# Kernel tuning notes

Hardware: AMD Instinct MI355X
Metric: run time of the kernel (lower is better)

The kernel has to match this reference:

```python
import jax, jax.numpy as jnp
import numpy as np

B, S, H = 4, 2048, 1024
NH, HD = 16, 64
WIN = 64  # window_size = min(64, seq_len)
SCALE = float(np.sqrt(HD))


def setup_inputs() -> dict:
    key = jax.random.key(0)
    ks = jax.random.split(key, 10)
    w = lambda k, shp: (jax.random.normal(k, shp, jnp.float32) * 0.02)
    return {
        "x": jax.random.normal(ks[0], (B, S, H), jnp.float32),
        "attention_mask": jnp.ones((B, S), jnp.int32),
        "Wq": w(ks[1], (H, NH * HD)), "bq": jnp.zeros((NH * HD,), jnp.float32),
        "Wk": w(ks[2], (H, NH * HD)), "bk": jnp.zeros((NH * HD,), jnp.float32),
        "Wv": w(ks[3], (H, NH * HD)), "bv": jnp.zeros((NH * HD,), jnp.float32),
        "Wo": w(ks[4], (NH * HD, H)), "bo": jnp.zeros((H,), jnp.float32),
    }


def reference(x, attention_mask, Wq, bq, Wk, bk, Wv, bv, Wo, bo):
    # projections -> [B, NH, S, HD]
    def split_heads(t):
        return t.reshape(B, S, NH, HD).transpose(0, 2, 1, 3)
    q = split_heads(x @ Wq + bq)
    k = split_heads(x @ Wk + bk)
    v = split_heads(x @ Wv + bv)

    scores = jnp.einsum("bhqd,bhkd->bhqk", q, k) / SCALE  # [B,NH,S,S]

    # local banded mask: |i - j| <= window_size // 2
    idx = jnp.arange(S)
    local = jnp.abs(idx[None, :] - idx[:, None]) <= (WIN // 2)  # [S,S]
    scores = jnp.where(local[None, None, :, :], scores, -jnp.inf)

    # padding mask: [B,1,1,S]
    scores = jnp.where(attention_mask[:, None, None, :] == 0, -jnp.inf, scores)

    probs = jax.nn.softmax(scores, axis=-1)
    probs = jnp.nan_to_num(probs)  # rows that are fully masked -> 0

    out = jnp.einsum("bhqk,bhkd->bhqd", probs, v)
    out = out.transpose(0, 2, 1, 3).reshape(B, S, NH * HD)
    return out @ Wo + bo
```

## Files before the change

kernel.cpp:

```cpp
#include <hip/hip_runtime.h>
#include <stdint.h>

typedef unsigned short u16;
typedef __attribute__((ext_vector_type(8))) short short8;
typedef __attribute__((ext_vector_type(4))) float f32x4;

#define S_LEN 2048
#define HID   1024
#define QKV_LD 3072
#define M_ROWS 8192

__device__ __forceinline__ u16 f2bf(float f) {
  unsigned u = __float_as_uint(f);
  unsigned r = (u + 0x7fffu + ((u >> 16) & 1u)) >> 16;
  return (u16)r;
}

__device__ __forceinline__ void gload16(const u16* g, u16* l) {
  __builtin_amdgcn_global_load_lds(
      (const __attribute__((address_space(1))) unsigned int*)(g),
      (__attribute__((address_space(3))) unsigned int*)(l),
      16, 0, 0);
}

__global__ __launch_bounds__(256) void cvt_f32_to_bf16(
    const float* __restrict__ in, u16* __restrict__ out, int n) {
  int i = (blockIdx.x * 256 + threadIdx.x) * 8;
  if (i + 8 > n) return;
  float4 a = *(const float4*)(in + i);
  float4 b = *(const float4*)(in + i + 4);
  u16 t[8];
  t[0] = f2bf(a.x); t[1] = f2bf(a.y); t[2] = f2bf(a.z); t[3] = f2bf(a.w);
  t[4] = f2bf(b.x); t[5] = f2bf(b.y); t[6] = f2bf(b.z); t[7] = f2bf(b.w);
  *(short8*)(out + i) = *(short8*)t;
}

__global__ __launch_bounds__(256) void transpose_to_bf16(
    const float* __restrict__ in, u16* __restrict__ out, int K, int N) {
  __shared__ float tile[32][33];
  int tx = threadIdx.x & 31, ty = threadIdx.x >> 5;
  int n0 = blockIdx.x * 32, k0 = blockIdx.y * 32;
#pragma unroll
  for (int i = 0; i < 32; i += 8)
    tile[ty + i][tx] = in[(size_t)(k0 + ty + i) * N + n0 + tx];
  __syncthreads();
#pragma unroll
  for (int i = 0; i < 32; i += 8)
    out[(size_t)(n0 + ty + i) * K + k0 + tx] = f2bf(tile[tx][ty + i]);
}

__global__ __launch_bounds__(256) void pack_bias(
    const float* __restrict__ bq, const float* __restrict__ bk,
    const float* __restrict__ bv, float* __restrict__ out) {
  int i = blockIdx.x * 256 + threadIdx.x;
  if (i >= 3072) return;
  out[i] = (i < 1024) ? bq[i] : (i < 2048) ? bk[i - 1024] : bv[i - 2048];
}

template<int OUT_BF16>
__global__ __launch_bounds__(256, 2) void gemm_bt(
    const u16* __restrict__ A, const u16* __restrict__ Bt,
    const float* __restrict__ bias, void* __restrict__ Cout,
    int M, int N, int K) {
  __shared__ __align__(16) u16 Al[128 * 64];
  __shared__ __align__(16) u16 Bl[128 * 64];
  const int tid = threadIdx.x;
  const int wave = tid >> 6, lane = tid & 63;
  const int nbn = N >> 7;
  int wg = blockIdx.x;
  const int cpx = (int)gridDim.x >> 3;
  wg = (wg & 7) * cpx + (wg >> 3);
  const int bm = wg / nbn, bn = wg % nbn;

  const int wm = wave >> 1, wn = wave & 1;
  const int lrow = lane >> 3;
  const int lslot = lane & 7;
  const int gslot = lslot ^ lrow;
  const int qlane = lane & 15, kgrp = lane >> 4;

  size_t a_off[4], b_off[4];
  u16 *al_base[4], *bl_base[4];
#pragma unroll
  for (int t = 0; t < 4; ++t) {
    int rr = (wave * 4 + t) * 8 + lrow;
    a_off[t] = (size_t)(bm * 128 + rr) * K + gslot * 8;
    b_off[t] = (size_t)(bn * 128 + rr) * K + gslot * 8;
    al_base[t] = Al + (wave * 4 + t) * 512;
    bl_base[t] = Bl + (wave * 4 + t) * 512;
  }

  f32x4 acc[4][4] = {};
  for (int kt = 0; kt < K; kt += 64) {
#pragma unroll
    for (int t = 0; t < 4; ++t) {
      gload16(A + a_off[t] + kt, al_base[t]);
      gload16(Bt + b_off[t] + kt, bl_base[t]);
    }
    __syncthreads();
#pragma unroll
    for (int kk = 0; kk < 2; ++kk) {
      short8 af[4], bf[4];
#pragma unroll
      for (int mf = 0; mf < 4; ++mf) {
        int row = wm * 64 + mf * 16 + qlane;
        int s = (kk * 4 + kgrp) ^ (row & 7);
        af[mf] = *(const short8*)&Al[row * 64 + s * 8];
      }
#pragma unroll
      for (int nf = 0; nf < 4; ++nf) {
        int row = wn * 64 + nf * 16 + qlane;
        int s = (kk * 4 + kgrp) ^ (row & 7);
        bf[nf] = *(const short8*)&Bl[row * 64 + s * 8];
      }
#pragma unroll
      for (int mf = 0; mf < 4; ++mf)
#pragma unroll
        for (int nf = 0; nf < 4; ++nf)
          acc[mf][nf] = __builtin_amdgcn_mfma_f32_16x16x32_bf16(
              af[mf], bf[nf], acc[mf][nf], 0, 0, 0);
    }
    __syncthreads();
  }

#pragma unroll
  for (int nf = 0; nf < 4; ++nf) {
    int col = bn * 128 + wn * 64 + nf * 16 + qlane;
    float bv = bias[col];
#pragma unroll
    for (int mf = 0; mf < 4; ++mf) {
      int row0 = bm * 128 + wm * 64 + mf * 16 + kgrp * 4;
#pragma unroll
      for (int r = 0; r < 4; ++r) {
        float v = acc[mf][nf][r] + bv;
        if (OUT_BF16)
          ((u16*)Cout)[(size_t)(row0 + r) * N + col] = f2bf(v);
        else
          ((float*)Cout)[(size_t)(row0 + r) * N + col] = v;
      }
    }
  }
}

__global__ __launch_bounds__(256, 2) void attn_local(
    const u16* __restrict__ qkv, const int* __restrict__ amask,
    u16* __restrict__ aout) {
  __shared__ __align__(16) u16 Kl[192][72];
  __shared__ __align__(16) u16 Vt[64][200];
  __shared__ __align__(16) u16 Pl[4][32][104];

  const int tid = threadIdx.x, wave = tid >> 6, lane = tid & 63;
  const int qlane = lane & 15, kgrp = lane >> 4;
  const int bz = blockIdx.x;
  const int qt = bz & 15, h = (bz >> 4) & 15, b = bz >> 8;
  const int qs0 = qt * 128;
  const int jt = qs0 - 32;
  const size_t rbase = (size_t)b * S_LEN;

  {
    const int r0 = tid >> 3, c0 = (tid & 7) * 8;
#pragma unroll
    for (int p = 0; p < 6; ++p) {
      int row = p * 32 + r0;
      int j = jt + row;
      u16 kv[8], vv[8];
      if (j >= 0 && j < S_LEN) {
        const u16* kp = qkv + (rbase + j) * QKV_LD + HID + h * 64 + c0;
        *(short8*)kv = *(const short8*)kp;
        *(short8*)vv = *(const short8*)(kp + HID);
      } else {
#pragma unroll
        for (int q = 0; q < 8; ++q) { kv[q] = 0; vv[q] = 0; }
      }
      *(short8*)&Kl[row][c0] = *(short8*)kv;
#pragma unroll
      for (int q = 0; q < 8; ++q) Vt[c0 + q][row] = vv[q];
    }
  }

  short8 qf[2][2];
#pragma unroll
  for (int mf = 0; mf < 2; ++mf)
#pragma unroll
    for (int kk = 0; kk < 2; ++kk)
      qf[mf][kk] = *(const short8*)(qkv +
          (rbase + qs0 + wave * 32 + mf * 16 + qlane) * QKV_LD +
          h * 64 + kk * 32 + kgrp * 8);

  __syncthreads();

  f32x4 sc[2][6] = {};
#pragma unroll
  for (int kk = 0; kk < 2; ++kk) {
    short8 kf[6];
#pragma unroll
    for (int nf = 0; nf < 6; ++nf)
      kf[nf] = *(const short8*)&Kl[wave * 32 + nf * 16 + qlane][kk * 32 + kgrp * 8];
#pragma unroll
    for (int mf = 0; mf < 2; ++mf)
#pragma unroll
      for (int nf = 0; nf < 6; ++nf)
        sc[mf][nf] = __builtin_amdgcn_mfma_f32_16x16x32_bf16(
            qf[mf][kk], kf[nf], sc[mf][nf], 0, 0, 0);
  }

  int jcol[6], mv[6];
#pragma unroll
  for (int nf = 0; nf < 6; ++nf) {
    int j = jt + wave * 32 + nf * 16 + qlane;
    jcol[nf] = j;
    mv[nf] = (j >= 0 && j < S_LEN) ? amask[rbase + j] : 0;
  }

  float inv[2][4];
#pragma unroll
  for (int mf = 0; mf < 2; ++mf) {
    const int irow0 = qs0 + wave * 32 + mf * 16 + kgrp * 4;
    float mx[4] = {-1e30f, -1e30f, -1e30f, -1e30f};
#pragma unroll
    for (int r = 0; r < 4; ++r) {
      int i = irow0 + r;
#pragma unroll
      for (int nf = 0; nf < 6; ++nf) {
        int d = i - jcol[nf];
        if (mv[nf] && d >= -32 && d <= 32) mx[r] = fmaxf(mx[r], sc[mf][nf][r]);
      }
    }
#pragma unroll
    for (int m = 1; m < 16; m <<= 1)
#pragma unroll
      for (int r = 0; r < 4; ++r)
        mx[r] = fmaxf(mx[r], __shfl_xor(mx[r], m));
    float sm[4] = {0.f, 0.f, 0.f, 0.f};
#pragma unroll
    for (int r = 0; r < 4; ++r) {
      int i = irow0 + r;
#pragma unroll
      for (int nf = 0; nf < 6; ++nf) {
        int d = i - jcol[nf];
        bool val = mv[nf] && d >= -32 && d <= 32;
        float p = val ? __expf((sc[mf][nf][r] - mx[r]) * 0.125f) : 0.f;
        sc[mf][nf][r] = p;
        sm[r] += p;
      }
    }
#pragma unroll
    for (int m = 1; m < 16; m <<= 1)
#pragma unroll
      for (int r = 0; r < 4; ++r)
        sm[r] += __shfl_xor(sm[r], m);
#pragma unroll
    for (int r = 0; r < 4; ++r)
      inv[mf][r] = sm[r] > 0.f ? 1.f / sm[r] : 0.f;
#pragma unroll
    for (int nf = 0; nf < 6; ++nf)
#pragma unroll
      for (int r = 0; r < 4; ++r)
        Pl[wave][mf * 16 + kgrp * 4 + r][nf * 16 + qlane] = f2bf(sc[mf][nf][r]);
  }
  __syncthreads();

  f32x4 oc[2][4] = {};
#pragma unroll
  for (int ks = 0; ks < 3; ++ks) {
    short8 pa[2], vb[4];
#pragma unroll
    for (int mf = 0; mf < 2; ++mf)
      pa[mf] = *(const short8*)&Pl[wave][mf * 16 + qlane][ks * 32 + kgrp * 8];
#pragma unroll
    for (int nf = 0; nf < 4; ++nf)
      vb[nf] = *(const short8*)&Vt[nf * 16 + qlane][wave * 32 + ks * 32 + kgrp * 8];
#pragma unroll
    for (int mf = 0; mf < 2; ++mf)
#pragma unroll
      for (int nf = 0; nf < 4; ++nf)
        oc[mf][nf] = __builtin_amdgcn_mfma_f32_16x16x32_bf16(
            pa[mf], vb[nf], oc[mf][nf], 0, 0, 0);
  }

#pragma unroll
  for (int mf = 0; mf < 2; ++mf)
#pragma unroll
    for (int nf = 0; nf < 4; ++nf)
#pragma unroll
      for (int r = 0; r < 4; ++r) {
        size_t row = rbase + qs0 + wave * 32 + mf * 16 + kgrp * 4 + r;
        aout[row * HID + h * 64 + nf * 16 + qlane] =
            f2bf(oc[mf][nf][r] * inv[mf][r]);
      }
}

extern "C" void kernel_launch(void* const* d_in, const int* in_sizes, int n_in,
                              void* d_out, int out_size, void* d_ws, size_t ws_size,
                              hipStream_t stream) {
  const float* x  = (const float*)d_in[0];
  const int* amask = (const int*)d_in[1];
  const float* Wq = (const float*)d_in[2];
  const float* bq = (const float*)d_in[3];
  const float* Wk = (const float*)d_in[4];
  const float* bk = (const float*)d_in[5];
  const float* Wv = (const float*)d_in[6];
  const float* bv = (const float*)d_in[7];
  const float* Wo = (const float*)d_in[8];
  const float* bo = (const float*)d_in[9];
  float* out = (float*)d_out;

  char* w = (char*)d_ws;
  u16* xb    = (u16*)w;   w += (size_t)M_ROWS * HID * 2;
  u16* wqkvt = (u16*)w;   w += (size_t)3072 * 1024 * 2;
  u16* wot   = (u16*)w;   w += (size_t)1024 * 1024 * 2;
  float* bqkv = (float*)w; w += 3072 * 4 + 256;
  u16* qkv   = (u16*)w;   w += (size_t)M_ROWS * 3072 * 2;
  u16* aout  = (u16*)w;   w += (size_t)M_ROWS * HID * 2;

  cvt_f32_to_bf16<<<4096, 256, 0, stream>>>(x, xb, M_ROWS * HID);
  dim3 tg(32, 32);
  transpose_to_bf16<<<tg, 256, 0, stream>>>(Wq, wqkvt,                1024, 1024);
  transpose_to_bf16<<<tg, 256, 0, stream>>>(Wk, wqkvt + 1024 * 1024,  1024, 1024);
  transpose_to_bf16<<<tg, 256, 0, stream>>>(Wv, wqkvt + 2048 * 1024,  1024, 1024);
  transpose_to_bf16<<<tg, 256, 0, stream>>>(Wo, wot,                  1024, 1024);
  pack_bias<<<12, 256, 0, stream>>>(bq, bk, bv, bqkv);

  gemm_bt<1><<<64 * 24, 256, 0, stream>>>(xb, wqkvt, bqkv, qkv, M_ROWS, 3072, 1024);
  attn_local<<<1024, 256, 0, stream>>>(qkv, amask, aout);
  gemm_bt<0><<<64 * 8, 256, 0, stream>>>(aout, wot, bo, out, M_ROWS, 1024, 1024);
}
```

Measured before the change: 131.7 us.

## Add specialised 256x384-tile QKV GEMM and merge preprocessing kernel launches

Replaces the generic QKV projection GEMM with a dedicated kernel that uses 512 threads, a 256x384 output tile, and a triple-buffered LDS pipeline with swizzled addressing and MFMA priority hints. This raises data reuse per block and overlaps global loads with compute. It also merges the four weight transposes into one 3D-grid launch and folds bias packing into the conversion kernel, cutting launch overhead. The 256-block grid fills the GPU in a single wave, which may leave compute units idle, and a large register footprint risks spills.

```diff
diff --git a/kernel.cpp b/kernel.cpp
--- a/kernel.cpp
+++ b/kernel.cpp
@@ -23,10 +23,22 @@
       16, 0, 0);
 }
 
-__global__ __launch_bounds__(256) void cvt_f32_to_bf16(
-    const float* __restrict__ in, u16* __restrict__ out, int n) {
+__device__ __forceinline__ void wgbar() {
+  asm volatile("" ::: "memory");
+  __builtin_amdgcn_s_barrier();
+  asm volatile("" ::: "memory");
+}
+
+__global__ __launch_bounds__(256) void cvt_bias(
+    const float* __restrict__ in, u16* __restrict__ out, int n,
+    const float* __restrict__ bq, const float* __restrict__ bk,
+    const float* __restrict__ bv, float* __restrict__ bqkv) {
+  if (blockIdx.x == (unsigned)(n / (256 * 8))) {
+    for (int i = threadIdx.x; i < 3072; i += 256)
+      bqkv[i] = (i < 1024) ? bq[i] : (i < 2048) ? bk[i - 1024] : bv[i - 2048];
+    return;
+  }
   int i = (blockIdx.x * 256 + threadIdx.x) * 8;
-  if (i + 8 > n) return;
   float4 a = *(const float4*)(in + i);
   float4 b = *(const float4*)(in + i + 4);
   u16 t[8];
@@ -35,26 +47,126 @@
   *(short8*)(out + i) = *(short8*)t;
 }
 
-__global__ __launch_bounds__(256) void transpose_to_bf16(
-    const float* __restrict__ in, u16* __restrict__ out, int K, int N) {
+__global__ __launch_bounds__(256) void pack_weights(
+    const float* __restrict__ Wq, const float* __restrict__ Wk,
+    const float* __restrict__ Wv, const float* __restrict__ Wo,
+    u16* __restrict__ wqkvt, u16* __restrict__ wot) {
   __shared__ float tile[32][33];
+  const int z = blockIdx.z;
+  const float* in = (z == 0) ? Wq : (z == 1) ? Wk : (z == 2) ? Wv : Wo;
+  u16* out = (z < 3) ? (wqkvt + (size_t)z * 1024 * 1024) : wot;
   int tx = threadIdx.x & 31, ty = threadIdx.x >> 5;
   int n0 = blockIdx.x * 32, k0 = blockIdx.y * 32;
 #pragma unroll
   for (int i = 0; i < 32; i += 8)
-    tile[ty + i][tx] = in[(size_t)(k0 + ty + i) * N + n0 + tx];
+    tile[ty + i][tx] = in[(size_t)(k0 + ty + i) * 1024 + n0 + tx];
   __syncthreads();
 #pragma unroll
   for (int i = 0; i < 32; i += 8)
-    out[(size_t)(n0 + ty + i) * K + k0 + tx] = f2bf(tile[tx][ty + i]);
-}
-
-__global__ __launch_bounds__(256) void pack_bias(
-    const float* __restrict__ bq, const float* __restrict__ bk,
-    const float* __restrict__ bv, float* __restrict__ out) {
-  int i = blockIdx.x * 256 + threadIdx.x;
-  if (i >= 3072) return;
-  out[i] = (i < 1024) ? bq[i] : (i < 2048) ? bk[i - 1024] : bv[i - 2048];
+    out[(size_t)(n0 + ty + i) * 1024 + k0 + tx] = f2bf(tile[tx][ty + i]);
+}
+
+__global__ __launch_bounds__(512, 2) void gemm_k1(
+    const u16* __restrict__ A, const u16* __restrict__ Bt,
+    const float* __restrict__ bias, u16* __restrict__ C) {
+  constexpr int K = 1024, NT = 32, N = 3072;
+  constexpr int SLOT = 20480;
+  constexpr int BOFF = 8192;
+  __shared__ __align__(16) u16 smem[3 * SLOT];
+
+  const int tid = threadIdx.x;
+  const int wave = tid >> 6, lane = tid & 63;
+  const int qlane = lane & 15, kgrp = lane >> 4;
+  const int wm = wave >> 2, wn = wave & 3;
+  int wg = blockIdx.x;
+  wg = (wg & 7) * 32 + (wg >> 3);
+  const int bm = wg >> 3, bn = wg & 7;
+
+  const int trp = tid >> 3, tp = tid & 7;
+  uint32_t aoff[2], boff[3];
+  int ldsA[2], ldsB[3];
+#pragma unroll
+  for (int i = 0; i < 2; ++i) {
+    int rp = i * 64 + trp, l = tp ^ (rp & 7);
+    int r = rp * 2 + (l >> 2), c8 = l & 3;
+    aoff[i] = (uint32_t)((bm * 256 + r) * K + c8 * 8);
+    ldsA[i] = i * 4096 + tid * 8;
+  }
+#pragma unroll
+  for (int i = 0; i < 3; ++i) {
+    int rp = i * 64 + trp, l = tp ^ (rp & 7);
+    int r = rp * 2 + (l >> 2), c8 = l & 3;
+    boff[i] = (uint32_t)((bn * 384 + r) * K + c8 * 8);
+    ldsB[i] = BOFF + i * 4096 + tid * 8;
+  }
+
+  int aaddr[8], baddr[6];
+#pragma unroll
+  for (int mf = 0; mf < 8; ++mf) {
+    int r = wm * 128 + mf * 16 + qlane;
+    aaddr[mf] = (r >> 1) * 64 + ((((r & 1) << 2) + kgrp) ^ ((r >> 1) & 7)) * 8;
+  }
+#pragma unroll
+  for (int nf = 0; nf < 6; ++nf) {
+    int r = wn * 96 + nf * 16 + qlane;
+    baddr[nf] = BOFF + (r >> 1) * 64 + ((((r & 1) << 2) + kgrp) ^ ((r >> 1) & 7)) * 8;
+  }
+
+  auto stg = [&](int t) {
+    u16* base = smem + (t % 3) * SLOT;
+#pragma unroll
+    for (int i = 0; i < 2; ++i)
+      gload16(A + aoff[i] + t * 32, base + ldsA[i]);
+#pragma unroll
+    for (int i = 0; i < 3; ++i)
+      gload16(Bt + boff[i] + t * 32, base + ldsB[i]);
+  };
+
+  f32x4 acc[8][6] = {};
+
+  stg(0);
+  stg(1);
+  asm volatile("s_waitcnt vmcnt(5)" ::: "memory");
+  wgbar();
+
+  for (int t = 0; t < NT; ++t) {
+    const u16* bp = smem + (t % 3) * SLOT;
+    short8 af[8];
+#pragma unroll
+    for (int mf = 0; mf < 8; ++mf)
+      af[mf] = *(const short8*)&bp[aaddr[mf]];
+    if (t + 2 < NT) stg(t + 2);
+#pragma unroll
+    for (int np = 0; np < 3; ++np) {
+      short8 bf0 = *(const short8*)&bp[baddr[np * 2]];
+      short8 bf1 = *(const short8*)&bp[baddr[np * 2 + 1]];
+      __builtin_amdgcn_s_setprio(1);
+#pragma unroll
+      for (int mf = 0; mf < 8; ++mf) {
+        acc[mf][np * 2] = __builtin_amdgcn_mfma_f32_16x16x32_bf16(
+            af[mf], bf0, acc[mf][np * 2], 0, 0, 0);
+        acc[mf][np * 2 + 1] = __builtin_amdgcn_mfma_f32_16x16x32_bf16(
+            af[mf], bf1, acc[mf][np * 2 + 1], 0, 0, 0);
+      }
+      __builtin_amdgcn_s_setprio(0);
+    }
+    if (t + 2 < NT)      asm volatile("s_waitcnt vmcnt(5)" ::: "memory");
+    else if (t + 1 < NT) asm volatile("s_waitcnt vmcnt(0)" ::: "memory");
+    if (t + 1 < NT) wgbar();
+  }
+
+#pragma unroll
+  for (int nf = 0; nf < 6; ++nf) {
+    int col = bn * 384 + wn * 96 + nf * 16 + qlane;
+    float bv = bias[col];
+#pragma unroll
+    for (int mf = 0; mf < 8; ++mf) {
+      int row0 = bm * 256 + wm * 128 + mf * 16 + kgrp * 4;
+#pragma unroll
+      for (int r = 0; r < 4; ++r)
+        C[(size_t)(row0 + r) * N + col] = f2bf(acc[mf][nf][r] + bv);
+    }
+  }
 }
 
 template<int OUT_BF16>
@@ -312,15 +424,10 @@
   u16* qkv   = (u16*)w;   w += (size_t)M_ROWS * 3072 * 2;
   u16* aout  = (u16*)w;   w += (size_t)M_ROWS * HID * 2;
 
-  cvt_f32_to_bf16<<<4096, 256, 0, stream>>>(x, xb, M_ROWS * HID);
-  dim3 tg(32, 32);
-  transpose_to_bf16<<<tg, 256, 0, stream>>>(Wq, wqkvt,                1024, 1024);
-  transpose_to_bf16<<<tg, 256, 0, stream>>>(Wk, wqkvt + 1024 * 1024,  1024, 1024);
-  transpose_to_bf16<<<tg, 256, 0, stream>>>(Wv, wqkvt + 2048 * 1024,  1024, 1024);
-  transpose_to_bf16<<<tg, 256, 0, stream>>>(Wo, wot,                  1024, 1024);
-  pack_bias<<<12, 256, 0, stream>>>(bq, bk, bv, bqkv);
-
-  gemm_bt<1><<<64 * 24, 256, 0, stream>>>(xb, wqkvt, bqkv, qkv, M_ROWS, 3072, 1024);
+  cvt_bias<<<4097, 256, 0, stream>>>(x, xb, M_ROWS * HID, bq, bk, bv, bqkv);
+  pack_weights<<<dim3(32, 32, 4), 256, 0, stream>>>(Wq, Wk, Wv, Wo, wqkvt, wot);
+
+  gemm_k1<<<256, 512, 0, stream>>>(xb, wqkvt, bqkv, qkv);
   attn_local<<<1024, 256, 0, stream>>>(qkv, amask, aout);
   gemm_bt<0><<<64 * 8, 256, 0, stream>>>(aout, wot, bo, out, M_ROWS, 1024, 1024);
 }
```

New measurement: 133.0 us. Within noise of the previous version (+1.0%).
